# Kernel tuning notes

Hardware: AMD Instinct MI355X
Metric: run time of the kernel (lower is better)

## Reference

```python
import jax, jax.numpy as jnp
import numpy as np

N_SAMPLE, N_ATOMS, N_TOKENS, N_CHAINS = 4, 8192, 1024, 8
AF3_THR = 1.1  # af3_clash_threshold
COUNT_THR = 100  # total_clash > 100
REL_THR = 0.5    # relative_clash > 0.5


def setup_inputs() -> dict:
    key = jax.random.key(0)
    k1, = jax.random.split(key, 1)
    # coords spread out a bit so clashes are sparse-ish but nonzero
    pred_coordinate = jax.random.normal(k1, (N_SAMPLE, N_ATOMS, 3), dtype=jnp.float32) * 5.0
    # balanced sorted chain assignment per token: guarantees all ids 0..N_CHAINS-1 present
    asym_id = ((jnp.arange(N_TOKENS) * N_CHAINS) // N_TOKENS).astype(jnp.int32)
    # monotone atoms -> tokens map (N_ATOMS // N_TOKENS atoms per token)
    atom_to_token_idx = (jnp.arange(N_ATOMS) // (N_ATOMS // N_TOKENS)).astype(jnp.int32)
    return {
        "pred_coordinate": pred_coordinate,
        "asym_id": asym_id,
        "atom_to_token_idx": atom_to_token_idx,
    }


def reference(pred_coordinate, asym_id, atom_to_token_idx):
    # Per-atom chain id, then one-hot chain membership M: [N_atoms, N_chains]
    atom_chain = asym_id[atom_to_token_idx]
    M = jax.nn.one_hot(atom_chain, N_CHAINS, dtype=pred_coordinate.dtype)
    n_per_chain = M.sum(axis=0)  # [C] atoms per chain

    # Squared pairwise distances via gram expansion (avoids [S,N,N,3] diff tensor)
    sq = jnp.sum(pred_coordinate * pred_coordinate, axis=-1)          # [S, N]
    gram = jnp.einsum('snd,smd->snm', pred_coordinate, pred_coordinate)  # [S, N, N]
    d2 = sq[:, :, None] + sq[:, None, :] - 2.0 * gram                 # [S, N, N]

    # dist < thr  <=>  d2 < thr^2 (both non-negative)
    clash = (d2 < AF3_THR * AF3_THR).astype(pred_coordinate.dtype)

    # counts[s, a, b] = #{(i in chain a, j in chain b) : clash}; two small GEMMs
    counts = jnp.einsum('snm,na,mb->sab', clash, M, M)  # [S, C, C]

    # original only fills strict off-diagonal pairs (i < j, mirrored); diagonal stays 0
    off = 1.0 - jnp.eye(N_CHAINS, dtype=counts.dtype)
    total = counts * off
    min_n = jnp.minimum(n_per_chain[:, None], n_per_chain[None, :])
    rel = total / min_n

    af3_clash_details = jnp.stack([total, rel], axis=-1)  # [S, C, C, 2]
    has_af3_clash = (total > COUNT_THR) | (rel > REL_THR)  # [S, C, C] bool
    return has_af3_clash, af3_clash_details
```

## Files before the change

### kernel.cpp

```cpp
#include <hip/hip_runtime.h>

#define NS 4
#define NA 8192
#define NTOK 1024
#define NC 8
#define THREADS 256
#define JSLOTS 4
#define JPB (THREADS * JSLOTS)
#define TI 128
#define NJB (NA / JPB)
#define NIB (NA / TI)


__global__ __launch_bounds__(THREADS)
void setup_kernel(const float* __restrict__ coords, const int* __restrict__ asym,
                  const int* __restrict__ a2t, float4* __restrict__ staged,
                  int* __restrict__ chain, int* __restrict__ counts) {
  const float THR2 = 1.21f;
  int idx = blockIdx.x * THREADS + threadIdx.x;
  float x = coords[3 * idx + 0], y = coords[3 * idx + 1], z = coords[3 * idx + 2];
  staged[idx] = make_float4(2.0f * x, 2.0f * y, 2.0f * z,
                            THR2 - (x * x + y * y + z * z));
  if (idx < NA) chain[idx] = asym[a2t[idx]];
  if (idx < NS * NC * NC) counts[idx] = 0;
}

__global__ __launch_bounds__(THREADS, 8)
void clash_kernel(const float* __restrict__ coords, const float4* __restrict__ staged,
                  const int* __restrict__ chain, int* __restrict__ counts) {
  __shared__ int tchain[TI];
  __shared__ int red[NC * NC];

  const int tid = threadIdx.x;
  const int ib = blockIdx.x, jb = blockIdx.y, s = blockIdx.z;
  if (tid < NC * NC) red[tid] = 0;

  const float* __restrict__ base = coords + (size_t)s * NA * 3;

  float xj[JSLOTS], yj[JSLOTS], zj[JSLOTS], tj[JSLOTS];
  int bj[JSLOTS];
#pragma unroll
  for (int u = 0; u < JSLOTS; ++u) {
    int j = jb * JPB + u * THREADS + tid;
    float x = base[3 * j + 0], y = base[3 * j + 1], z = base[3 * j + 2];
    xj[u] = x; yj[u] = y; zj[u] = z;
    tj[u] = x * x + y * y + z * z;
    bj[u] = chain[j];
  }
  if (tid < TI) tchain[tid] = chain[ib * TI + tid];
  __syncthreads();

  int uni_a = __syncthreads_and(tchain[tid & (TI - 1)] == tchain[0]);

  const float4* __restrict__ tg = staged + (size_t)s * NA + ib * TI;

  if (uni_a) {
    int acc[JSLOTS];
#pragma unroll
    for (int u = 0; u < JSLOTS; ++u) acc[u] = 0;
#pragma unroll 8
    for (int t = 0; t < TI; ++t) {
      float4 ci = tg[t];
#pragma unroll
      for (int u = 0; u < JSLOTS; ++u) {
        float d = fmaf(ci.x, xj[u], fmaf(ci.y, yj[u], fmaf(ci.z, zj[u], ci.w)));
        acc[u] += (d > tj[u]);
      }
    }
    const int A = tchain[0];
#pragma unroll
    for (int u = 0; u < JSLOTS; ++u) {
      int v = acc[u];
      int b0 = __builtin_amdgcn_readfirstlane(bj[u]);
      if (__all(bj[u] == b0)) {
#pragma unroll
        for (int m = 32; m >= 1; m >>= 1) v += __shfl_xor(v, m, 64);
        if ((tid & 63) == 0 && v) atomicAdd(&red[A * NC + b0], v);
      } else if (v) {
        atomicAdd(&red[A * NC + bj[u]], v);
      }
    }
  } else {
    for (int t = 0; t < TI; ++t) {
      int a = tchain[t];
      float4 ci = tg[t];
#pragma unroll
      for (int u = 0; u < JSLOTS; ++u) {
        float d = fmaf(ci.x, xj[u], fmaf(ci.y, yj[u], fmaf(ci.z, zj[u], ci.w)));
        if (d > tj[u]) atomicAdd(&red[a * NC + bj[u]], 1);
      }
    }
  }

  __syncthreads();
  if (tid < NC * NC) {
    int v = red[tid];
    if (v) atomicAdd(&counts[s * NC * NC + tid], v);
  }
}

__global__ __launch_bounds__(THREADS)
void finalize_kernel(const int* __restrict__ asym, const int* __restrict__ counts,
                     float* __restrict__ out) {
  __shared__ int hist[NC];
  int tid = threadIdx.x;
  if (tid < NC) hist[tid] = 0;
  __syncthreads();
  for (int t = tid; t < NTOK; t += THREADS) atomicAdd(&hist[asym[t]], NA / NTOK);
  __syncthreads();

  int c = counts[tid];
  int a = (tid >> 3) & 7, b = tid & 7;
  float total = (a == b) ? 0.0f : (float)c;
  float minn = (float)min(hist[a], hist[b]);
  float rel = total / minn;
  out[tid] = ((total > 100.0f) || (rel > 0.5f)) ? 1.0f : 0.0f;
  out[256 + 2 * tid + 0] = total;
  out[256 + 2 * tid + 1] = rel;
}

extern "C" void kernel_launch(void* const* d_in, const int* in_sizes, int n_in,
                              void* d_out, int out_size, void* d_ws, size_t ws_size,
                              hipStream_t stream) {
  const float* coords = (const float*)d_in[0];
  const int* asym = (const int*)d_in[1];
  const int* a2t = (const int*)d_in[2];
  float* out = (float*)d_out;

  float4* staged = (float4*)d_ws;
  int* chain = (int*)(staged + NS * NA);
  int* counts = chain + NA;

  setup_kernel<<<dim3(NS * NA / THREADS), THREADS, 0, stream>>>(coords, asym, a2t,
                                                                staged, chain, counts);
  clash_kernel<<<dim3(NIB, NJB, NS), THREADS, 0, stream>>>(coords, staged, chain, counts);
  finalize_kernel<<<1, THREADS, 0, stream>>>(asym, counts, out);
}
```

Measured before the change: 96.16 us.

## Exploit pair symmetry with triangular tiling and skip same-chain tiles

Instead of a full 2D grid over i and j blocks, the clash kernel now runs over a flattened lower-triangular set of tiles. Counts from strictly off-diagonal tiles are mirrored into the transposed chain pair. Tiles where every i and j atom belongs to the same chain exit early, since diagonal chain pairs are zeroed in the output anyway. The j coordinates now come from the staged float4 buffer, and the uniform-chain path counts with ballot plus popcount instead of a shuffle reduction. Together these roughly halve the pairwise arithmetic, at the cost of a serial loop to decode the tile index and a small rounding change in the threshold comparison.

```diff
diff --git a/kernel.cpp b/kernel.cpp
--- a/kernel.cpp
+++ b/kernel.cpp
@@ -7,9 +7,9 @@
 #define THREADS 256
 #define JSLOTS 4
 #define JPB (THREADS * JSLOTS)
-#define TI 128
-#define NJB (NA / JPB)
-#define NIB (NA / TI)
+#define TI 64
+#define TPJ (JPB / TI)
+#define GRIDX 576
 
 
 __global__ __launch_bounds__(THREADS)
@@ -26,68 +26,86 @@
 }
 
 __global__ __launch_bounds__(THREADS, 8)
-void clash_kernel(const float* __restrict__ coords, const float4* __restrict__ staged,
-                  const int* __restrict__ chain, int* __restrict__ counts) {
+void clash_kernel(const float4* __restrict__ staged, const int* __restrict__ chain,
+                  int* __restrict__ counts) {
   __shared__ int tchain[TI];
   __shared__ int red[NC * NC];
 
   const int tid = threadIdx.x;
-  const int ib = blockIdx.x, jb = blockIdx.y, s = blockIdx.z;
+  const int s = blockIdx.z;
+
+  int f = blockIdx.x, jb = 0;
+  while (f >= (jb + 1) * TPJ) { f -= (jb + 1) * TPJ; ++jb; }
+  const int ib = f;
+  const bool strict = ib < jb * TPJ;
+
   if (tid < NC * NC) red[tid] = 0;
 
-  const float* __restrict__ base = coords + (size_t)s * NA * 3;
+  const float4* __restrict__ sb = staged + (size_t)s * NA;
+  const float THR2 = 1.21f;
 
-  float xj[JSLOTS], yj[JSLOTS], zj[JSLOTS], tj[JSLOTS];
+  float xj[JSLOTS], yj[JSLOTS], zj[JSLOTS], tj2[JSLOTS];
   int bj[JSLOTS];
 #pragma unroll
   for (int u = 0; u < JSLOTS; ++u) {
     int j = jb * JPB + u * THREADS + tid;
-    float x = base[3 * j + 0], y = base[3 * j + 1], z = base[3 * j + 2];
-    xj[u] = x; yj[u] = y; zj[u] = z;
-    tj[u] = x * x + y * y + z * z;
+    float4 cj = sb[j];
+    xj[u] = cj.x; yj[u] = cj.y; zj[u] = cj.z;
+    tj2[u] = 2.0f * (THR2 - cj.w);
     bj[u] = chain[j];
   }
   if (tid < TI) tchain[tid] = chain[ib * TI + tid];
   __syncthreads();
 
-  int uni_a = __syncthreads_and(tchain[tid & (TI - 1)] == tchain[0]);
+  const int A = tchain[0];
+  int uni_i = (tchain[tid & (TI - 1)] == A);
+  if (__syncthreads_and(uni_i && bj[0] == A && bj[1] == A && bj[2] == A && bj[3] == A))
+    return;
+  int uni_a = __syncthreads_and(uni_i);
 
-  const float4* __restrict__ tg = staged + (size_t)s * NA + ib * TI;
+  const float4* __restrict__ tg = sb + ib * TI;
 
-  if (uni_a) {
-    int acc[JSLOTS];
+  int b0[JSLOTS];
+  bool scalar_ok = uni_a;
 #pragma unroll
-    for (int u = 0; u < JSLOTS; ++u) acc[u] = 0;
+  for (int u = 0; u < JSLOTS; ++u) {
+    b0[u] = __builtin_amdgcn_readfirstlane(bj[u]);
+    scalar_ok = scalar_ok && __all(bj[u] == b0[u]);
+  }
+
+  if (scalar_ok) {
+    int acc[JSLOTS] = {0, 0, 0, 0};
 #pragma unroll 8
     for (int t = 0; t < TI; ++t) {
       float4 ci = tg[t];
+      float w2 = ci.w + ci.w;
 #pragma unroll
       for (int u = 0; u < JSLOTS; ++u) {
-        float d = fmaf(ci.x, xj[u], fmaf(ci.y, yj[u], fmaf(ci.z, zj[u], ci.w)));
-        acc[u] += (d > tj[u]);
+        float d = fmaf(ci.x, xj[u], fmaf(ci.y, yj[u], fmaf(ci.z, zj[u], w2)));
+        acc[u] += __popcll(__ballot(d > tj2[u]));
       }
     }
-    const int A = tchain[0];
+    if ((tid & 63) == 0) {
 #pragma unroll
-    for (int u = 0; u < JSLOTS; ++u) {
-      int v = acc[u];
-      int b0 = __builtin_amdgcn_readfirstlane(bj[u]);
-      if (__all(bj[u] == b0)) {
-#pragma unroll
-        for (int m = 32; m >= 1; m >>= 1) v += __shfl_xor(v, m, 64);
-        if ((tid & 63) == 0 && v) atomicAdd(&red[A * NC + b0], v);
-      } else if (v) {
-        atomicAdd(&red[A * NC + bj[u]], v);
+      for (int u = 0; u < JSLOTS; ++u) {
+        if (acc[u]) {
+          atomicAdd(&red[A * NC + b0[u]], acc[u]);
+          if (strict) atomicAdd(&red[b0[u] * NC + A], acc[u]);
+        }
       }
     }
   } else {
     for (int t = 0; t < TI; ++t) {
+      float4 ci = tg[t];
       int a = tchain[t];
-      float4 ci = tg[t];
+      float w2 = ci.w + ci.w;
 #pragma unroll
       for (int u = 0; u < JSLOTS; ++u) {
-        float d = fmaf(ci.x, xj[u], fmaf(ci.y, yj[u], fmaf(ci.z, zj[u], ci.w)));
-        if (d > tj[u]) atomicAdd(&red[a * NC + bj[u]], 1);
+        float d = fmaf(ci.x, xj[u], fmaf(ci.y, yj[u], fmaf(ci.z, zj[u], w2)));
+        if (d > tj2[u]) {
+          atomicAdd(&red[a * NC + bj[u]], 1);
+          if (strict) atomicAdd(&red[bj[u] * NC + a], 1);
+        }
       }
     }
   }
@@ -133,6 +151,6 @@
 
   setup_kernel<<<dim3(NS * NA / THREADS), THREADS, 0, stream>>>(coords, asym, a2t,
                                                                 staged, chain, counts);
-  clash_kernel<<<dim3(NIB, NJB, NS), THREADS, 0, stream>>>(coords, staged, chain, counts);
+  clash_kernel<<<dim3(GRIDX, 1, NS), THREADS, 0, stream>>>(staged, chain, counts);
   finalize_kernel<<<1, THREADS, 0, stream>>>(asym, counts, out);
 }
```

Measured after the change: 80.43 us. 16.4% less time.
